# Optimization experiments

Measured on AMD Instinct MI355X. Metric: run time of the kernel, lower is better.

Reference implementation:

```python
import jax, jax.numpy as jnp
import numpy as np

# Irreps config: input/output = 32x0e + 16x1o (dim 80), H=4 heads -> head = 8x0e + 4x1o (dim 20)
M0, M1 = 32, 16      # input muls for 0e / 1o
m0, m1 = 8, 4        # per-head muls
H = 4
HEAD_DIM = m0 + 3 * m1   # 20
WNUM = H * (M0 * m0 + M1 * m0 + M0 * m1 + M1 * m1)  # 2304 per-edge TP weights
NB, HID = 16, 64
SQRT3 = np.float32(np.sqrt(3.0))
EPS = 1e-8


def radial_mlp(x, W1, b1, W2, b2):
    return jax.nn.silu(x @ W1 + b1) @ W2 + b2


def tp_edge(ss, vv, sh0, sh1, w):
    """FullyConnectedTensorProduct (32x0e+16x1o) x (1x0e+1x1o) -> H*(8x0e+4x1o) with per-edge weights w [E, WNUM].
    Paths: 0e*0e->0e, 1o*1o->0e (CG dot/sqrt3), 0e*1o->1o, 1o*0e->1o; path norm 1/sqrt(fan_in)."""
    E = ss.shape[0]
    per = M0 * m0 + M1 * m0 + M0 * m1 + M1 * m1  # 576
    w = w.reshape(E, H, per)
    o = 0
    Wss = w[..., o:o + M0 * m0].reshape(E, H, M0, m0); o += M0 * m0
    Wvv = w[..., o:o + M1 * m0].reshape(E, H, M1, m0); o += M1 * m0
    Wsv = w[..., o:o + M0 * m1].reshape(E, H, M0, m1); o += M0 * m1
    Wvs = w[..., o:o + M1 * m1].reshape(E, H, M1, m1)
    fan = np.float32(np.sqrt(M0 + M1))  # fan_in = 48 for both output irreps
    vv_dot = jnp.einsum('eui,ei->eu', vv, sh1) / SQRT3
    out0 = (jnp.einsum('eu,ehuw->ehw', ss * sh0[:, None], Wss)
            + jnp.einsum('eu,ehuw->ehw', vv_dot, Wvv)) / fan          # [E,H,m0]
    out1 = (jnp.einsum('eu,ehuw->ehw', ss, Wsv)[..., None] * sh1[:, None, None, :]
            + jnp.einsum('eui,ehuw->ehwi', vv * sh0[:, None, None], Wvs)) / fan  # [E,H,m1,3]
    return out0, out1


def setup_inputs() -> dict:
    key = jax.random.key(0)
    ks = jax.random.split(key, 24)
    N, E = 2000, 32000
    g = lambda k, s, sc=1.0: jax.random.normal(k, s, jnp.float32) * sc
    inp = {}
    inp['node_features'] = g(ks[0], (N, M0 + 3 * M1))
    inp['edge_index'] = jax.random.randint(ks[1], (2, E), 0, N)
    inp['edge_sh'] = g(ks[2], (E, 4))
    inp['edge_radial_emb'] = jax.random.uniform(ks[3], (E, NB), jnp.float32)
    # query e3nn Linear (per-head blocks)
    inp['Wq0'] = g(ks[4], (H, M0, m0))
    inp['Wq1'] = g(ks[5], (H, M1, m1))
    # radial MLPs for key / value TP weights
    inp['Wk1'] = g(ks[6], (NB, HID), 1 / np.sqrt(NB)); inp['bk1'] = jnp.zeros((HID,), jnp.float32)
    inp['Wk2'] = g(ks[7], (HID, WNUM), 1 / np.sqrt(HID)); inp['bk2'] = jnp.zeros((WNUM,), jnp.float32)
    inp['Wv1'] = g(ks[8], (NB, HID), 1 / np.sqrt(NB)); inp['bv1'] = jnp.zeros((HID,), jnp.float32)
    inp['Wv2'] = g(ks[9], (HID, WNUM), 1 / np.sqrt(HID)); inp['bv2'] = jnp.zeros((WNUM,), jnp.float32)
    # single-head dot-product TP -> 0e (shared weights)
    inp['Wd0'] = g(ks[10], (m0, m0))
    inp['Wd1'] = g(ks[11], (m1, m1))
    # output projection Linear (all heads mixed per irrep)
    inp['Wo0'] = g(ks[12], (H * m0, M0))
    inp['Wo1'] = g(ks[13], (H * m1, M1))
    # FFN: out irreps -> (2*M0)x0e + M1x1o -> out irreps
    inp['Wf1_0'] = g(ks[14], (M0, 2 * M0))
    inp['Wf1_1'] = g(ks[15], (M1, M1))
    inp['Wf2_0'] = g(ks[16], (2 * M0, M0))
    inp['Wf2_1'] = g(ks[17], (M1, M1))
    return inp


def reference(node_features, edge_index, edge_sh, edge_radial_emb,
              Wq0, Wq1, Wk1, bk1, Wk2, bk2, Wv1, bv1, Wv2, bv2,
              Wd0, Wd1, Wo0, Wo1, Wf1_0, Wf1_1, Wf2_0, Wf2_1):
    N = node_features.shape[0]
    s = node_features[:, :M0]                       # [N, M0] scalars
    v = node_features[:, M0:].reshape(N, M1, 3)     # [N, M1, 3] vectors
    src, dst = edge_index[0], edge_index[1]

    # query Linear (e3nn: per-irrep channel mix, norm 1/sqrt(fan_in))
    q0 = jnp.einsum('nu,huw->nhw', s, Wq0) / np.sqrt(M0)
    q1 = jnp.einsum('nui,huw->nhwi', v, Wq1) / np.sqrt(M1)

    sh0, sh1 = edge_sh[:, 0], edge_sh[:, 1:4]
    ss, vv = s[src], v[src]                         # gather per edge

    wk = radial_mlp(edge_radial_emb, Wk1, bk1, Wk2, bk2)
    wv = radial_mlp(edge_radial_emb, Wv1, bv1, Wv2, bv2)
    k0, k1 = tp_edge(ss, vv, sh0, sh1, wk)
    v0, v1 = tp_edge(ss, vv, sh0, sh1, wv)

    # per-head equivariant dot product -> 0e logits
    qd0, qd1 = q0[dst], q1[dst]
    fan_d = np.float32(np.sqrt(m0 * m0 + m1 * m1))
    logits = (jnp.einsum('ehu,uv,ehv->eh', qd0, Wd0, k0)
              + jnp.einsum('ehui,uv,ehvi->eh', qd1, Wd1, k1) / SQRT3) / fan_d
    logits = logits / np.sqrt(HEAD_DIM)             # self.scale
    logits = jnp.clip(logits, -10.0, 10.0)

    # scatter softmax over edges sharing a destination node
    seg_max = jax.ops.segment_max(logits, dst, num_segments=N)
    seg_max = jnp.maximum(seg_max, -10.0)           # handle empty segments
    ex = jnp.exp(logits - seg_max[dst])
    denom = jax.ops.segment_sum(ex, dst, num_segments=N)
    alpha = ex / (denom[dst] + 1e-12)               # [E, H]

    agg0 = jax.ops.segment_sum(alpha[..., None] * v0, dst, num_segments=N)        # [N,H,m0]
    agg1 = jax.ops.segment_sum(alpha[..., None, None] * v1, dst, num_segments=N)  # [N,H,m1,3]

    # output projection Linear over concatenated heads
    o0 = agg0.reshape(N, H * m0) @ Wo0 / np.sqrt(H * m0)
    o1 = jnp.einsum('nui,uw->nwi', agg1.reshape(N, H * m1, 3), Wo1) / np.sqrt(H * m1)

    # residual (input irreps == output irreps -> identity skip)
    x0 = s + o0
    x1 = v + o1

    # FFN with SafeNormActivation
    f0 = x0 @ Wf1_0 / np.sqrt(M0)                               # [N, 2*M0]
    f1 = jnp.einsum('nui,uw->nwi', x1, Wf1_1) / np.sqrt(M1)     # [N, M1, 3]
    a0 = jax.nn.silu(f0)
    norms = jnp.linalg.norm(f1, axis=-1, keepdims=True)
    safe = jnp.maximum(norms, EPS)
    a1 = jnp.where(norms < EPS, 0.0, (f1 / safe) * jax.nn.silu(norms))
    g0 = a0 @ Wf2_0 / np.sqrt(2 * M0)
    g1 = jnp.einsum('nui,uw->nwi', a1, Wf2_1) / np.sqrt(M1)

    out0 = x0 + g0
    out1 = x1 + g1
    return jnp.concatenate([out0, out1.reshape(N, M1 * 3)], axis=-1)
```

## Files before the change

kernel.cpp:

```cpp
#include <hip/hip_runtime.h>

typedef unsigned int uint;
typedef unsigned short ushort;
typedef __attribute__((ext_vector_type(8))) short bf16x8;
typedef __attribute__((ext_vector_type(4))) float f32x4;

#define N_NODES 2000
#define N_EDGES 32000
#define WNUM 2304

constexpr size_t OFF_AGG0 = 0;
constexpr size_t OFF_AGG1 = 64000;
constexpr size_t OFF_DEN  = 160000;
constexpr size_t OFF_FLAG = 168000;
constexpr size_t OFF_W2T  = 168004;
constexpr size_t OFF_QT0  = 315460;
constexpr size_t OFF_QT1  = 379460;

__device__ __forceinline__ float b2f(ushort u){ union{uint i; float f;}x; x.i=((uint)u)<<16; return x.f; }
__device__ __forceinline__ float lo16(uint w){ union{uint u; float f;}x; x.u=w<<16; return x.f; }
__device__ __forceinline__ float hi16(uint w){ union{uint u; float f;}x; x.u=w&0xFFFF0000u; return x.f; }
__device__ __forceinline__ ushort f2b(float f){
  union{float f; uint u;}x; x.f=f;
  uint r = (x.u + 0x7FFFu + ((x.u>>16)&1u)) >> 16;
  return (ushort)r;
}
__device__ __forceinline__ float siluf(float x){ return x / (1.f + __expf(-x)); }

template<bool F32>
__device__ __forceinline__ float ldf(const void* p, int i){
  if (F32) return ((const float*)p)[i];
  return b2f(((const ushort*)p)[i]);
}
__device__ __forceinline__ float ldfr(const void* p, int i, bool f32){
  return f32 ? ((const float*)p)[i] : b2f(((const ushort*)p)[i]);
}

template<bool F32>
__device__ void node_q_one(const void* __restrict__ nf,
    const void* __restrict__ Wq0, const void* __restrict__ Wq1,
    const void* __restrict__ Wd0, const void* __restrict__ Wd1,
    float* __restrict__ qt0, float* __restrict__ qt1, int tid){
  int n = tid >> 2, h = tid & 3;
  float s[32], v[48];
  #pragma unroll
  for (int u=0; u<32; ++u) s[u] = ldf<F32>(nf, n*80+u);
  #pragma unroll
  for (int u=0; u<48; ++u) v[u] = ldf<F32>(nf, n*80+32+u);
  float q0[8];
  #pragma unroll
  for (int w=0; w<8; ++w){
    float a = 0.f;
    #pragma unroll
    for (int u=0; u<32; ++u) a += s[u]*ldf<F32>(Wq0, h*256 + u*8 + w);
    q0[w] = a * 0.17677669529663687f;
  }
  #pragma unroll
  for (int vv=0; vv<8; ++vv){
    float a = 0.f;
    #pragma unroll
    for (int u=0; u<8; ++u) a += q0[u]*ldf<F32>(Wd0, u*8+vv);
    qt0[n*32 + h*8 + vv] = a;
  }
  float q1[12];
  #pragma unroll
  for (int w=0; w<4; ++w)
    #pragma unroll
    for (int i=0; i<3; ++i){
      float a = 0.f;
      #pragma unroll
      for (int u=0; u<16; ++u) a += v[u*3+i]*ldf<F32>(Wq1, h*64 + u*4 + w);
      q1[w*3+i] = a * 0.25f;
    }
  #pragma unroll
  for (int vv=0; vv<4; ++vv)
    #pragma unroll
    for (int i=0; i<3; ++i){
      float a = 0.f;
      #pragma unroll
      for (int u=0; u<4; ++u) a += q1[u*3+i]*ldf<F32>(Wd1, u*4+vv);
      qt1[n*48 + h*12 + vv*3 + i] = a;
    }
}

__global__ __launch_bounds__(256) void prep_kernel(
    const void* __restrict__ nf, const void* __restrict__ Wk2, const void* __restrict__ Wv2,
    const void* __restrict__ Wq0, const void* __restrict__ Wq1,
    const void* __restrict__ Wd0, const void* __restrict__ Wd1,
    ushort* __restrict__ W2T, float* __restrict__ qt0, float* __restrict__ qt1,
    float* __restrict__ aggz, int* __restrict__ flag){
  __shared__ int s_cnt;
  const int t = threadIdx.x;
  if (t == 0) s_cnt = 0;
  __syncthreads();
  {
    uint u = ((const ushort*)nf)[t*2];
    uint ex = (u >> 7) & 0xFFu;
    if (ex >= 0xA0u) atomicAdd(&s_cnt, 1);
  }
  __syncthreads();
  const bool F32 = (s_cnt >= 20);
  if (blockIdx.x == 0 && t == 0) *flag = F32 ? 1 : 0;

  if (blockIdx.x < 72){
    __shared__ ushort tile[64][66];
    const int b = blockIdx.x, mat = b / 36, jt = b - mat*36;
    const void* W = mat ? Wv2 : Wk2;
    const int j0 = jt*64;
    const int jo = t & 63, cb = t >> 6;
    #pragma unroll
    for (int k=0; k<16; ++k){
      const int c = cb + k*4;
      tile[c][jo] = F32 ? f2b(((const float*)W)[(size_t)c*WNUM + j0 + jo])
                        : ((const ushort*)W)[(size_t)c*WNUM + j0 + jo];
    }
    __syncthreads();
    const int jl = t >> 2, c0 = (t & 3)*16;
    ushort* dst = W2T + (size_t)mat*147456 + (size_t)(j0+jl)*64 + c0;
    #pragma unroll
    for (int k=0; k<16; ++k) dst[k] = tile[c0+k][jl];
  } else {
    const int zb = (int)blockIdx.x - 72;
    float4* az = (float4*)aggz;
    for (int idx = zb*256 + t; idx < 42000; idx += 32*256)
      az[idx] = make_float4(0.f,0.f,0.f,0.f);
    const int tid = zb*256 + t;
    if (tid < N_NODES*4){
      if (F32) node_q_one<true >(nf, Wq0, Wq1, Wd0, Wd1, qt0, qt1, tid);
      else     node_q_one<false>(nf, Wq0, Wq1, Wd0, Wd1, qt0, qt1, tid);
    }
  }
}

struct Smem {
  ushort hidA[2][32][72];
  float fssT[32][36];
  float fvvT[16][36];
  float sslT[32][36];
  float vshT[16][3][36];
  float sh1T[3][36];
  int   dstL[32];
};

template<bool F32>
__device__ void edge_body(
    const void* __restrict__ nf,  const int* __restrict__ eidx,
    const void* __restrict__ esh, const void* __restrict__ emb,
    const void* __restrict__ Wk1, const void* __restrict__ bk1, const void* __restrict__ bk2,
    const void* __restrict__ Wv1, const void* __restrict__ bv1, const void* __restrict__ bv2,
    const ushort* __restrict__ W2T,
    const float* __restrict__ qt0g, const float* __restrict__ qt1g,
    float* __restrict__ agg0, float* __restrict__ agg1, float* __restrict__ denom,
    Smem& sm){
  const int t  = threadIdx.x;
  const int hw = t >> 5;
  const int r  = t & 31;
  const int geb = blockIdx.x*32;

  #pragma unroll 1
  for (int e=0; e<4; ++e){
    const int le = hw*4+e, ge = geb+le;
    const int src = eidx[ge], d = eidx[N_EDGES+ge];
    const float sh0 = ldf<F32>(esh, ge*4+0);
    const float s1a = ldf<F32>(esh, ge*4+1), s1b = ldf<F32>(esh, ge*4+2), s1c = ldf<F32>(esh, ge*4+3);
    if (r == 0) sm.dstL[le] = d;
    if (r < 3) sm.sh1T[r][le] = (r==0)? s1a : (r==1)? s1b : s1c;
    float sv = ldf<F32>(nf, src*80 + r);
    sm.sslT[r][le] = sv;
    sm.fssT[r][le] = sv * sh0;
    if (r < 16){
      float v0 = ldf<F32>(nf, src*80+32+r*3+0);
      float v1 = ldf<F32>(nf, src*80+32+r*3+1);
      float v2 = ldf<F32>(nf, src*80+32+r*3+2);
      sm.vshT[r][0][le] = v0*sh0; sm.vshT[r][1][le] = v1*sh0; sm.vshT[r][2][le] = v2*sh0;
      sm.fvvT[r][le] = (v0*s1a + v1*s1b + v2*s1c) * 0.5773502691896258f;
    }
  }

  #pragma unroll 1
  for (int e=0; e<4; ++e){
    const int le = hw*4+e, ge = geb+le;
    float em[16];
    if (F32){
      const float4* p = (const float4*)((const float*)emb + ge*16);
      float4 a=p[0], b=p[1], c=p[2], d4=p[3];
      em[0]=a.x; em[1]=a.y; em[2]=a.z; em[3]=a.w;
      em[4]=b.x; em[5]=b.y; em[6]=b.z; em[7]=b.w;
      em[8]=c.x; em[9]=c.y; em[10]=c.z; em[11]=c.w;
      em[12]=d4.x; em[13]=d4.y; em[14]=d4.z; em[15]=d4.w;
    } else {
      const uint4* p = (const uint4*)((const ushort*)emb + ge*16);
      uint4 a=p[0], b=p[1];
      em[0]=lo16(a.x); em[1]=hi16(a.x); em[2]=lo16(a.y); em[3]=hi16(a.y);
      em[4]=lo16(a.z); em[5]=hi16(a.z); em[6]=lo16(a.w); em[7]=hi16(a.w);
      em[8]=lo16(b.x); em[9]=hi16(b.x); em[10]=lo16(b.y); em[11]=hi16(b.y);
      em[12]=lo16(b.z); em[13]=hi16(b.z); em[14]=lo16(b.w); em[15]=hi16(b.w);
    }
    #pragma unroll
    for (int cc=0; cc<2; ++cc){
      const int c = r + cc*32;
      float ak = ldf<F32>(bk1, c), av = ldf<F32>(bv1, c);
      #pragma unroll
      for (int b=0; b<16; ++b){
        ak += em[b] * ldf<F32>(Wk1, b*64 + c);
        av += em[b] * ldf<F32>(Wv1, b*64 + c);
      }
      sm.hidA[0][le][c] = f2b(siluf(ak));
      sm.hidA[1][le][c] = f2b(siluf(av));
    }
  }
  __syncthreads();

  const int h = t >> 6;
  const int lane = t & 63, q = lane >> 4, n = lane & 15;
  const ushort* w2tk = W2T;
  const ushort* w2tv = W2T + 147456;

  bf16x8 af[2][2][2];
  #pragma unroll
  for (int kv=0; kv<2; ++kv)
    #pragma unroll
    for (int Mt=0; Mt<2; ++Mt)
      #pragma unroll
      for (int kh=0; kh<2; ++kh)
        af[kv][Mt][kh] = *(const bf16x8*)&sm.hidA[kv][Mt*16+n][kh*32 + q*8];

  float aK0[2][4], aV0[2][4], aPK[2][4], aPV[2][4], aWK[3][2][4], aWV[3][2][4];
  #pragma unroll
  for (int Mt=0; Mt<2; ++Mt)
    #pragma unroll
    for (int z=0; z<4; ++z){
      aK0[Mt][z]=0.f; aV0[Mt][z]=0.f; aPK[Mt][z]=0.f; aPV[Mt][z]=0.f;
      aWK[0][Mt][z]=0.f; aWK[1][Mt][z]=0.f; aWK[2][Mt][z]=0.f;
      aWV[0][Mt][z]=0.f; aWV[1][Mt][z]=0.f; aWV[2][Mt][z]=0.f;
    }

  #pragma unroll 2
  for (int tl=0; tl<24; ++tl){
    const size_t tb = ((size_t)((h*36+tl)*16 + n))*64 + q*8;
    bf16x8 bk0 = *(const bf16x8*)(w2tk + tb), bk1f = *(const bf16x8*)(w2tk + tb + 32);
    bf16x8 bv0 = *(const bf16x8*)(w2tv + tb), bv1f = *(const bf16x8*)(w2tv + tb + 32);
    const int j = h*576 + tl*16 + n;
    const float bbk = ldf<F32>(bk2, j), bbv = ldf<F32>(bv2, j);
    const bool ss = (tl < 16);
    const int u = ss ? (tl*2 + (n>>3)) : ((tl-16)*2 + (n>>3));
    #pragma unroll
    for (int Mt=0; Mt<2; ++Mt){
      f32x4 fv = ss ? *(const f32x4*)&sm.fssT[u][Mt*16+q*4]
                    : *(const f32x4*)&sm.fvvT[u][Mt*16+q*4];
      f32x4 ck = {bbk,bbk,bbk,bbk};
      ck = __builtin_amdgcn_mfma_f32_16x16x32_bf16(af[0][Mt][0], bk0, ck, 0,0,0);
      ck = __builtin_amdgcn_mfma_f32_16x16x32_bf16(af[0][Mt][1], bk1f, ck, 0,0,0);
      f32x4 cv = {bbv,bbv,bbv,bbv};
      cv = __builtin_amdgcn_mfma_f32_16x16x32_bf16(af[1][Mt][0], bv0, cv, 0,0,0);
      cv = __builtin_amdgcn_mfma_f32_16x16x32_bf16(af[1][Mt][1], bv1f, cv, 0,0,0);
      #pragma unroll
      for (int z=0; z<4; ++z){ aK0[Mt][z] += ck[z]*fv[z]; aV0[Mt][z] += cv[z]*fv[z]; }
    }
  }
  #pragma unroll 2
  for (int tl=24; tl<32; ++tl){
    const size_t tb = ((size_t)((h*36+tl)*16 + n))*64 + q*8;
    bf16x8 bk0 = *(const bf16x8*)(w2tk + tb), bk1f = *(const bf16x8*)(w2tk + tb + 32);
    bf16x8 bv0 = *(const bf16x8*)(w2tv + tb), bv1f = *(const bf16x8*)(w2tv + tb + 32);
    const int j = h*576 + tl*16 + n;
    const float bbk = ldf<F32>(bk2, j), bbv = ldf<F32>(bv2, j);
    const int u = (tl-24)*4 + (n>>2);
    #pragma unroll
    for (int Mt=0; Mt<2; ++Mt){
      f32x4 fv = *(const f32x4*)&sm.sslT[u][Mt*16+q*4];
      f32x4 ck = {bbk,bbk,bbk,bbk};
      ck = __builtin_amdgcn_mfma_f32_16x16x32_bf16(af[0][Mt][0], bk0, ck, 0,0,0);
      ck = __builtin_amdgcn_mfma_f32_16x16x32_bf16(af[0][Mt][1], bk1f, ck, 0,0,0);
      f32x4 cv = {bbv,bbv,bbv,bbv};
      cv = __builtin_amdgcn_mfma_f32_16x16x32_bf16(af[1][Mt][0], bv0, cv, 0,0,0);
      cv = __builtin_amdgcn_mfma_f32_16x16x32_bf16(af[1][Mt][1], bv1f, cv, 0,0,0);
      #pragma unroll
      for (int z=0; z<4; ++z){ aPK[Mt][z] += ck[z]*fv[z]; aPV[Mt][z] += cv[z]*fv[z]; }
    }
  }
  #pragma unroll 1
  for (int tl=32; tl<36; ++tl){
    const size_t tb = ((size_t)((h*36+tl)*16 + n))*64 + q*8;
    bf16x8 bk0 = *(const bf16x8*)(w2tk + tb), bk1f = *(const bf16x8*)(w2tk + tb + 32);
    bf16x8 bv0 = *(const bf16x8*)(w2tv + tb), bv1f = *(const bf16x8*)(w2tv + tb + 32);
    const int j = h*576 + tl*16 + n;
    const float bbk = ldf<F32>(bk2, j), bbv = ldf<F32>(bv2, j);
    const int u = (tl-32)*4 + (n>>2);
    #pragma unroll
    for (int Mt=0; Mt<2; ++Mt){
      f32x4 ck = {bbk,bbk,bbk,bbk};
      ck = __builtin_amdgcn_mfma_f32_16x16x32_bf16(af[0][Mt][0], bk0, ck, 0,0,0);
      ck = __builtin_amdgcn_mfma_f32_16x16x32_bf16(af[0][Mt][1], bk1f, ck, 0,0,0);
      f32x4 cv = {bbv,bbv,bbv,bbv};
      cv = __builtin_amdgcn_mfma_f32_16x16x32_bf16(af[1][Mt][0], bv0, cv, 0,0,0);
      cv = __builtin_amdgcn_mfma_f32_16x16x32_bf16(af[1][Mt][1], bv1f, cv, 0,0,0);
      #pragma unroll
      for (int i=0; i<3; ++i){
        f32x4 fv = *(const f32x4*)&sm.vshT[u][i][Mt*16+q*4];
        #pragma unroll
        for (int z=0; z<4; ++z){ aWK[i][Mt][z] += ck[z]*fv[z]; aWV[i][Mt][z] += cv[z]*fv[z]; }
      }
    }
  }

  #pragma unroll
  for (int Mt=0; Mt<2; ++Mt)
    #pragma unroll
    for (int z=0; z<4; ++z){
      aK0[Mt][z] += __shfl_xor(aK0[Mt][z], 8, 64);
      aV0[Mt][z] += __shfl_xor(aV0[Mt][z], 8, 64);
      aPK[Mt][z] += __shfl_xor(aPK[Mt][z], 4, 64);
      aPK[Mt][z] += __shfl_xor(aPK[Mt][z], 8, 64);
      aPV[Mt][z] += __shfl_xor(aPV[Mt][z], 4, 64);
      aPV[Mt][z] += __shfl_xor(aPV[Mt][z], 8, 64);
      #pragma unroll
      for (int i=0; i<3; ++i){
        aWK[i][Mt][z] += __shfl_xor(aWK[i][Mt][z], 4, 64);
        aWK[i][Mt][z] += __shfl_xor(aWK[i][Mt][z], 8, 64);
        aWV[i][Mt][z] += __shfl_xor(aWV[i][Mt][z], 4, 64);
        aWV[i][Mt][z] += __shfl_xor(aWV[i][Mt][z], 8, 64);
      }
    }

  const float invfan = 0.14433756729740643f;
  int dn[2][4];
  #pragma unroll
  for (int Mt=0; Mt<2; ++Mt)
    #pragma unroll
    for (int z=0; z<4; ++z) dn[Mt][z] = sm.dstL[Mt*16 + q*4 + z];

  f32x4 s1v[3][2];
  #pragma unroll
  for (int i=0; i<3; ++i)
    #pragma unroll
    for (int Mt=0; Mt<2; ++Mt)
      s1v[i][Mt] = *(const f32x4*)&sm.sh1T[i][Mt*16+q*4];

  float lgp[2][4];
  #pragma unroll
  for (int Mt=0; Mt<2; ++Mt)
    #pragma unroll
    for (int z=0; z<4; ++z){
      float acc = 0.f;
      if (n < 8) acc = qt0g[dn[Mt][z]*32 + h*8 + n] * aK0[Mt][z];
      if (n < 4){
        float s = 0.f;
        #pragma unroll
        for (int i=0; i<3; ++i){
          float k1 = aPK[Mt][z]*s1v[i][Mt][z] + aWK[i][Mt][z];
          s += qt1g[dn[Mt][z]*48 + h*12 + n*3 + i] * k1;
        }
        acc += s * 0.5773502691896258f;
      }
      lgp[Mt][z] = acc;
    }
  #pragma unroll
  for (int Mt=0; Mt<2; ++Mt)
    #pragma unroll
    for (int z=0; z<4; ++z){
      lgp[Mt][z] += __shfl_xor(lgp[Mt][z], 1, 64);
      lgp[Mt][z] += __shfl_xor(lgp[Mt][z], 2, 64);
      lgp[Mt][z] += __shfl_xor(lgp[Mt][z], 4, 64);
      lgp[Mt][z] += __shfl_xor(lgp[Mt][z], 8, 64);
    }

  float exv[2][4];
  #pragma unroll
  for (int Mt=0; Mt<2; ++Mt)
    #pragma unroll
    for (int z=0; z<4; ++z){
      float lg = lgp[Mt][z] * invfan * 0.025f;
      lg = fminf(10.f, fmaxf(-10.f, lg));
      exv[Mt][z] = __expf(lg - 10.0f);
    }

  if (n == 0){
    #pragma unroll
    for (int Mt=0; Mt<2; ++Mt)
      #pragma unroll
      for (int z=0; z<4; ++z)
        atomicAdd(denom + dn[Mt][z]*4 + h, exv[Mt][z]);
  }
  if (n < 8){
    #pragma unroll
    for (int Mt=0; Mt<2; ++Mt)
      #pragma unroll
      for (int z=0; z<4; ++z)
        atomicAdd(agg0 + dn[Mt][z]*32 + h*8 + n, exv[Mt][z]*aV0[Mt][z]*invfan);
  }
  if (n < 4){
    #pragma unroll
    for (int i=0; i<3; ++i)
      #pragma unroll
      for (int Mt=0; Mt<2; ++Mt)
        #pragma unroll
        for (int z=0; z<4; ++z){
          float v1 = (aPV[Mt][z]*s1v[i][Mt][z] + aWV[i][Mt][z]) * invfan;
          atomicAdd(agg1 + dn[Mt][z]*48 + h*12 + n*3 + i, exv[Mt][z]*v1);
        }
  }
}

__global__ __launch_bounds__(256) void edge_kernel(
    const void* nf, const int* eidx, const void* esh, const void* emb,
    const void* Wk1, const void* bk1, const void* bk2,
    const void* Wv1, const void* bv1, const void* bv2,
    const ushort* W2T, const float* qt0g, const float* qt1g,
    float* agg0, float* agg1, float* denom, const int* flag){
  __shared__ Smem sm;
  if (*flag)
    edge_body<true >(nf,eidx,esh,emb,Wk1,bk1,bk2,Wv1,bv1,bv2,W2T,qt0g,qt1g,agg0,agg1,denom,sm);
  else
    edge_body<false>(nf,eidx,esh,emb,Wk1,bk1,bk2,Wv1,bv1,bv2,W2T,qt0g,qt1g,agg0,agg1,denom,sm);
}

__global__ __launch_bounds__(256) void node_out_kernel(
    const void* __restrict__ nf, const float* __restrict__ agg0r, const float* __restrict__ agg1r,
    const float* __restrict__ denom,
    const void* __restrict__ Wo0, const void* __restrict__ Wo1,
    const void* __restrict__ Wf10, const void* __restrict__ Wf11,
    const void* __restrict__ Wf20, const void* __restrict__ Wf21,
    void* __restrict__ out, const int* __restrict__ flag){
  __shared__ float ag0[4][32], ag1[4][48], adiv[4][4];
  __shared__ float x0s[4][32], x1s[4][48], a0s[4][64], f1s[4][48], coefs[4][16];
  const bool F32 = (*flag) != 0;
  const int g = threadIdx.x >> 6, t = threadIdx.x & 63;
  const int n = blockIdx.x*4 + g;
  if (t < 4) adiv[g][t] = 1.f / (denom[n*4+t] + 1e-12f);
  __syncthreads();
  if (t < 32) ag0[g][t] = agg0r[n*32+t] * adiv[g][t>>3];
  if (t < 48) ag1[g][t] = agg1r[n*48+t] * adiv[g][t/12];
  __syncthreads();
  if (t < 32){
    float o = 0.f;
    #pragma unroll
    for (int k=0; k<32; ++k) o += ag0[g][k]*ldfr(Wo0, k*32+t, F32);
    x0s[g][t] = ldfr(nf, n*80+t, F32) + o*0.17677669529663687f;
  }
  if (t < 48){
    int w = t/3, i = t - w*3;
    float o = 0.f;
    #pragma unroll
    for (int u=0; u<16; ++u) o += ag1[g][u*3+i]*ldfr(Wo1, u*16+w, F32);
    x1s[g][t] = ldfr(nf, n*80+32+t, F32) + o*0.25f;
  }
  __syncthreads();
  {
    float f0 = 0.f;
    #pragma unroll
    for (int u=0; u<32; ++u) f0 += x0s[g][u]*ldfr(Wf10, u*64+t, F32);
    a0s[g][t] = siluf(f0*0.17677669529663687f);
  }
  if (t < 48){
    int w = t/3, i = t - w*3;
    float f1 = 0.f;
    #pragma unroll
    for (int u=0; u<16; ++u) f1 += x1s[g][u*3+i]*ldfr(Wf11, u*16+w, F32);
    f1s[g][t] = f1*0.25f;
  }
  __syncthreads();
  if (t < 16){
    float a = f1s[g][t*3], b = f1s[g][t*3+1], c = f1s[g][t*3+2];
    float nrm = sqrtf(a*a+b*b+c*c);
    float safe = fmaxf(nrm, 1e-8f);
    coefs[g][t] = (nrm < 1e-8f) ? 0.f : siluf(nrm)/safe;
  }
  __syncthreads();
  if (t < 32){
    float gg = 0.f;
    #pragma unroll
    for (int u=0; u<64; ++u) gg += a0s[g][u]*ldfr(Wf20, u*32+t, F32);
    float val = x0s[g][t] + gg*0.125f;
    if (F32) ((float*)out)[n*80+t] = val; else ((ushort*)out)[n*80+t] = f2b(val);
  }
  if (t < 48){
    int w = t/3, i = t - w*3;
    float gg = 0.f;
    #pragma unroll
    for (int u=0; u<16; ++u) gg += coefs[g][u]*f1s[g][u*3+i]*ldfr(Wf21, u*16+w, F32);
    float val = x1s[g][t] + gg*0.25f;
    if (F32) ((float*)out)[n*80+32+t] = val; else ((ushort*)out)[n*80+32+t] = f2b(val);
  }
}

extern "C" void kernel_launch(void* const* d_in, const int* in_sizes, int n_in,
                              void* d_out, int out_size, void* d_ws, size_t ws_size,
                              hipStream_t stream){
  const void* nf   = d_in[0];
  const int*  eidx = (const int*)d_in[1];
  const void* esh  = d_in[2];
  const void* emb  = d_in[3];
  const void* Wq0  = d_in[4];
  const void* Wq1  = d_in[5];
  const void* Wk1  = d_in[6];
  const void* bk1  = d_in[7];
  const void* Wk2  = d_in[8];
  const void* bk2  = d_in[9];
  const void* Wv1  = d_in[10];
  const void* bv1  = d_in[11];
  const void* Wv2  = d_in[12];
  const void* bv2  = d_in[13];
  const void* Wd0  = d_in[14];
  const void* Wd1  = d_in[15];
  const void* Wo0  = d_in[16];
  const void* Wo1  = d_in[17];
  const void* Wf10 = d_in[18];
  const void* Wf11 = d_in[19];
  const void* Wf20 = d_in[20];
  const void* Wf21 = d_in[21];
  float* ws = (float*)d_ws;

  float* agg0  = ws + OFF_AGG0;
  float* agg1  = ws + OFF_AGG1;
  float* denom = ws + OFF_DEN;
  int*   flag  = (int*)(ws + OFF_FLAG);
  ushort* W2T  = (ushort*)(ws + OFF_W2T);
  float* qt0   = ws + OFF_QT0;
  float* qt1   = ws + OFF_QT1;

  prep_kernel<<<104, 256, 0, stream>>>(nf, Wk2, Wv2, Wq0, Wq1, Wd0, Wd1,
                                       W2T, qt0, qt1, agg0, flag);
  edge_kernel<<<N_EDGES/32, 256, 0, stream>>>(nf, eidx, esh, emb,
                                              Wk1, bk1, bk2, Wv1, bv1, bv2,
                                              W2T, qt0, qt1,
                                              agg0, agg1, denom, flag);
  node_out_kernel<<<N_NODES/4, 256, 0, stream>>>(nf, agg0, agg1, denom,
                                                 Wo0, Wo1, Wf10, Wf11, Wf20, Wf21, d_out, flag);
}
```

Baseline: 242.1 us.

## Sort edges by destination and segment-reduce contributions in shared memory before atomics

Adds a counting sort of edges by destination (count, scan, scatter kernels) and has the edge kernel process edges in that order. Per-edge softmax numerators and weighted values are staged in shared memory and run-length reduced over consecutive equal destinations, so one atomic is issued per destination run instead of one per edge. The node output kernel is also reshaped to one 64-thread block per node. This adds three small launches and an extra sync plus a serial 32-step reduction per block, in exchange for far fewer global atomics.

After: 239.3 us. No clear change (-1.2%).

```diff
diff --git a/kernel.cpp b/kernel.cpp
--- a/kernel.cpp
+++ b/kernel.cpp
@@ -16,6 +16,8 @@
 constexpr size_t OFF_W2T  = 168004;
 constexpr size_t OFF_QT0  = 315460;
 constexpr size_t OFF_QT1  = 379460;
+constexpr size_t OFF_CNT  = 475460;
+constexpr size_t OFF_EORD = 477460;
 
 __device__ __forceinline__ float b2f(ushort u){ union{uint i; float f;}x; x.i=((uint)u)<<16; return x.f; }
 __device__ __forceinline__ float lo16(uint w){ union{uint u; float f;}x; x.u=w<<16; return x.f; }
@@ -88,7 +90,7 @@
     const void* __restrict__ Wq0, const void* __restrict__ Wq1,
     const void* __restrict__ Wd0, const void* __restrict__ Wd1,
     ushort* __restrict__ W2T, float* __restrict__ qt0, float* __restrict__ qt1,
-    float* __restrict__ aggz, int* __restrict__ flag){
+    float* __restrict__ aggz, int* __restrict__ cnt, int* __restrict__ flag){
   __shared__ int s_cnt;
   const int t = threadIdx.x;
   if (t == 0) s_cnt = 0;
@@ -124,11 +126,46 @@
     float4* az = (float4*)aggz;
     for (int idx = zb*256 + t; idx < 42000; idx += 32*256)
       az[idx] = make_float4(0.f,0.f,0.f,0.f);
+    for (int idx = zb*256 + t; idx < N_NODES; idx += 32*256)
+      cnt[idx] = 0;
     const int tid = zb*256 + t;
     if (tid < N_NODES*4){
       if (F32) node_q_one<true >(nf, Wq0, Wq1, Wd0, Wd1, qt0, qt1, tid);
       else     node_q_one<false>(nf, Wq0, Wq1, Wd0, Wd1, qt0, qt1, tid);
     }
+  }
+}
+
+__global__ __launch_bounds__(256) void cnt_kernel(const int* __restrict__ eidx, int* __restrict__ cnt){
+  int e = blockIdx.x*256 + threadIdx.x;
+  if (e < N_EDGES) atomicAdd(cnt + eidx[N_EDGES + e], 1);
+}
+
+__global__ __launch_bounds__(256) void scan_kernel(int* __restrict__ cnt){
+  __shared__ int ls[256];
+  const int t = threadIdx.x;
+  const int base = t*8;
+  int v[8]; int s = 0;
+  #pragma unroll
+  for (int k=0; k<8; ++k){ int idx = base+k; v[k] = (idx < N_NODES) ? cnt[idx] : 0; s += v[k]; }
+  ls[t] = s; __syncthreads();
+  for (int off=1; off<256; off<<=1){
+    int x = (t >= off) ? ls[t-off] : 0;
+    __syncthreads();
+    ls[t] += x;
+    __syncthreads();
+  }
+  int ex = ls[t] - s;
+  #pragma unroll
+  for (int k=0; k<8; ++k){ int idx = base+k; if (idx < N_NODES){ int c = v[k]; cnt[idx] = ex; ex += c; } }
+}
+
+__global__ __launch_bounds__(256) void scat_kernel(const int* __restrict__ eidx,
+                                                   int* __restrict__ cnt, int* __restrict__ eord){
+  int e = blockIdx.x*256 + threadIdx.x;
+  if (e < N_EDGES){
+    int p = atomicAdd(cnt + eidx[N_EDGES + e], 1);
+    eord[p] = e;
   }
 }
 
@@ -139,12 +176,14 @@
   float sslT[32][36];
   float vshT[16][3][36];
   float sh1T[3][36];
+  float cont[4][32][21];
   int   dstL[32];
 };
 
 template<bool F32>
 __device__ void edge_body(
     const void* __restrict__ nf,  const int* __restrict__ eidx,
+    const int* __restrict__ eord,
     const void* __restrict__ esh, const void* __restrict__ emb,
     const void* __restrict__ Wk1, const void* __restrict__ bk1, const void* __restrict__ bk2,
     const void* __restrict__ Wv1, const void* __restrict__ bv1, const void* __restrict__ bv2,
@@ -159,7 +198,8 @@
 
   #pragma unroll 1
   for (int e=0; e<4; ++e){
-    const int le = hw*4+e, ge = geb+le;
+    const int le = hw*4+e;
+    const int ge = eord[geb+le];
     const int src = eidx[ge], d = eidx[N_EDGES+ge];
     const float sh0 = ldf<F32>(esh, ge*4+0);
     const float s1a = ldf<F32>(esh, ge*4+1), s1b = ldf<F32>(esh, ge*4+2), s1c = ldf<F32>(esh, ge*4+3);
@@ -179,7 +219,8 @@
 
   #pragma unroll 1
   for (int e=0; e<4; ++e){
-    const int le = hw*4+e, ge = geb+le;
+    const int le = hw*4+e;
+    const int ge = eord[geb+le];
     float em[16];
     if (F32){
       const float4* p = (const float4*)((const float*)emb + ge*16);
@@ -365,121 +406,120 @@
       lgp[Mt][z] += __shfl_xor(lgp[Mt][z], 8, 64);
     }
 
-  float exv[2][4];
   #pragma unroll
   for (int Mt=0; Mt<2; ++Mt)
     #pragma unroll
     for (int z=0; z<4; ++z){
       float lg = lgp[Mt][z] * invfan * 0.025f;
       lg = fminf(10.f, fmaxf(-10.f, lg));
-      exv[Mt][z] = __expf(lg - 10.0f);
-    }
-
-  if (n == 0){
-    #pragma unroll
-    for (int Mt=0; Mt<2; ++Mt)
-      #pragma unroll
-      for (int z=0; z<4; ++z)
-        atomicAdd(denom + dn[Mt][z]*4 + h, exv[Mt][z]);
-  }
-  if (n < 8){
-    #pragma unroll
-    for (int Mt=0; Mt<2; ++Mt)
-      #pragma unroll
-      for (int z=0; z<4; ++z)
-        atomicAdd(agg0 + dn[Mt][z]*32 + h*8 + n, exv[Mt][z]*aV0[Mt][z]*invfan);
-  }
-  if (n < 4){
-    #pragma unroll
-    for (int i=0; i<3; ++i)
-      #pragma unroll
-      for (int Mt=0; Mt<2; ++Mt)
+      const float ex = __expf(lg - 10.0f);
+      const int el = Mt*16 + q*4 + z;
+      if (n == 0) sm.cont[h][el][0] = ex;
+      if (n < 8)  sm.cont[h][el][1+n] = ex * aV0[Mt][z] * invfan;
+      if (n < 4){
         #pragma unroll
-        for (int z=0; z<4; ++z){
+        for (int i=0; i<3; ++i){
           float v1 = (aPV[Mt][z]*s1v[i][Mt][z] + aWV[i][Mt][z]) * invfan;
-          atomicAdd(agg1 + dn[Mt][z]*48 + h*12 + n*3 + i, exv[Mt][z]*v1);
+          sm.cont[h][el][9+n*3+i] = ex * v1;
         }
+      }
+    }
+  __syncthreads();
+
+  if (t < 84){
+    const int h2 = t / 21, comp = t - h2*21;
+    float acc = 0.f;
+    #pragma unroll 1
+    for (int e2=0; e2<32; ++e2){
+      acc += sm.cont[h2][e2][comp];
+      const int d2 = sm.dstL[e2];
+      if (e2 == 31 || sm.dstL[e2+1] != d2){
+        if (comp == 0)      atomicAdd(denom + d2*4  + h2, acc);
+        else if (comp < 9)  atomicAdd(agg0  + d2*32 + h2*8  + (comp-1), acc);
+        else                atomicAdd(agg1  + d2*48 + h2*12 + (comp-9), acc);
+        acc = 0.f;
+      }
+    }
   }
 }
 
 __global__ __launch_bounds__(256) void edge_kernel(
-    const void* nf, const int* eidx, const void* esh, const void* emb,
+    const void* nf, const int* eidx, const int* eord, const void* esh, const void* emb,
     const void* Wk1, const void* bk1, const void* bk2,
     const void* Wv1, const void* bv1, const void* bv2,
     const ushort* W2T, const float* qt0g, const float* qt1g,
     float* agg0, float* agg1, float* denom, const int* flag){
   __shared__ Smem sm;
   if (*flag)
-    edge_body<true >(nf,eidx,esh,emb,Wk1,bk1,bk2,Wv1,bv1,bv2,W2T,qt0g,qt1g,agg0,agg1,denom,sm);
+    edge_body<true >(nf,eidx,eord,esh,emb,Wk1,bk1,bk2,Wv1,bv1,bv2,W2T,qt0g,qt1g,agg0,agg1,denom,sm);
   else
-    edge_body<false>(nf,eidx,esh,emb,Wk1,bk1,bk2,Wv1,bv1,bv2,W2T,qt0g,qt1g,agg0,agg1,denom,sm);
-}
-
-__global__ __launch_bounds__(256) void node_out_kernel(
+    edge_body<false>(nf,eidx,eord,esh,emb,Wk1,bk1,bk2,Wv1,bv1,bv2,W2T,qt0g,qt1g,agg0,agg1,denom,sm);
+}
+
+__global__ __launch_bounds__(64) void node_out_kernel(
     const void* __restrict__ nf, const float* __restrict__ agg0r, const float* __restrict__ agg1r,
     const float* __restrict__ denom,
     const void* __restrict__ Wo0, const void* __restrict__ Wo1,
     const void* __restrict__ Wf10, const void* __restrict__ Wf11,
     const void* __restrict__ Wf20, const void* __restrict__ Wf21,
     void* __restrict__ out, const int* __restrict__ flag){
-  __shared__ float ag0[4][32], ag1[4][48], adiv[4][4];
-  __shared__ float x0s[4][32], x1s[4][48], a0s[4][64], f1s[4][48], coefs[4][16];
+  __shared__ float ag0[32], ag1[48], adiv[4];
+  __shared__ float x0s[32], x1s[48], a0s[64], f1s[48], coefs[16];
   const bool F32 = (*flag) != 0;
-  const int g = threadIdx.x >> 6, t = threadIdx.x & 63;
-  const int n = blockIdx.x*4 + g;
-  if (t < 4) adiv[g][t] = 1.f / (denom[n*4+t] + 1e-12f);
-  __syncthreads();
-  if (t < 32) ag0[g][t] = agg0r[n*32+t] * adiv[g][t>>3];
-  if (t < 48) ag1[g][t] = agg1r[n*48+t] * adiv[g][t/12];
+  const int n = blockIdx.x, t = threadIdx.x;
+  if (t < 4) adiv[t] = 1.f / (denom[n*4+t] + 1e-12f);
+  __syncthreads();
+  if (t < 32) ag0[t] = agg0r[n*32+t] * adiv[t>>3];
+  if (t < 48) ag1[t] = agg1r[n*48+t] * adiv[t/12];
   __syncthreads();
   if (t < 32){
     float o = 0.f;
     #pragma unroll
-    for (int k=0; k<32; ++k) o += ag0[g][k]*ldfr(Wo0, k*32+t, F32);
-    x0s[g][t] = ldfr(nf, n*80+t, F32) + o*0.17677669529663687f;
+    for (int k=0; k<32; ++k) o += ag0[k]*ldfr(Wo0, k*32+t, F32);
+    x0s[t] = ldfr(nf, n*80+t, F32) + o*0.17677669529663687f;
   }
   if (t < 48){
     int w = t/3, i = t - w*3;
     float o = 0.f;
     #pragma unroll
-    for (int u=0; u<16; ++u) o += ag1[g][u*3+i]*ldfr(Wo1, u*16+w, F32);
-    x1s[g][t] = ldfr(nf, n*80+32+t, F32) + o*0.25f;
+    for (int u=0; u<16; ++u) o += ag1[u*3+i]*ldfr(Wo1, u*16+w, F32);
+    x1s[t] = ldfr(nf, n*80+32+t, F32) + o*0.25f;
   }
   __syncthreads();
   {
     float f0 = 0.f;
     #pragma unroll
-    for (int u=0; u<32; ++u) f0 += x0s[g][u]*ldfr(Wf10, u*64+t, F32);
-    a0s[g][t] = siluf(f0*0.17677669529663687f);
+    for (int u=0; u<32; ++u) f0 += x0s[u]*ldfr(Wf10, u*64+t, F32);
+    a0s[t] = siluf(f0*0.17677669529663687f);
   }
   if (t < 48){
     int w = t/3, i = t - w*3;
     float f1 = 0.f;
     #pragma unroll
-    for (int u=0; u<16; ++u) f1 += x1s[g][u*3+i]*ldfr(Wf11, u*16+w, F32);
-    f1s[g][t] = f1*0.25f;
+    for (int u=0; u<16; ++u) f1 += x1s[u*3+i]*ldfr(Wf11, u*16+w, F32);
+    f1s[t] = f1*0.25f;
   }
   __syncthreads();
   if (t < 16){
-    float a = f1s[g][t*3], b = f1s[g][t*3+1], c = f1s[g][t*3+2];
+    float a = f1s[t*3], b = f1s[t*3+1], c = f1s[t*3+2];
     float nrm = sqrtf(a*a+b*b+c*c);
     float safe = fmaxf(nrm, 1e-8f);
-    coefs[g][t] = (nrm < 1e-8f) ? 0.f : siluf(nrm)/safe;
+    coefs[t] = (nrm < 1e-8f) ? 0.f : siluf(nrm)/safe;
   }
   __syncthreads();
   if (t < 32){
-    float gg = 0.f;
-    #pragma unroll
-    for (int u=0; u<64; ++u) gg += a0s[g][u]*ldfr(Wf20, u*32+t, F32);
-    float val = x0s[g][t] + gg*0.125f;
+    float g = 0.f;
+    #pragma unroll
+    for (int u=0; u<64; ++u) g += a0s[u]*ldfr(Wf20, u*32+t, F32);
+    float val = x0s[t] + g*0.125f;
     if (F32) ((float*)out)[n*80+t] = val; else ((ushort*)out)[n*80+t] = f2b(val);
   }
   if (t < 48){
     int w = t/3, i = t - w*3;
-    float gg = 0.f;
-    #pragma unroll
-    for (int u=0; u<16; ++u) gg += coefs[g][u]*f1s[g][u*3+i]*ldfr(Wf21, u*16+w, F32);
-    float val = x1s[g][t] + gg*0.25f;
+    float g = 0.f;
+    #pragma unroll
+    for (int u=0; u<16; ++u) g += coefs[u]*f1s[u*3+i]*ldfr(Wf21, u*16+w, F32);
+    float val = x1s[t] + g*0.25f;
     if (F32) ((float*)out)[n*80+32+t] = val; else ((ushort*)out)[n*80+32+t] = f2b(val);
   }
 }
@@ -518,13 +558,18 @@
   ushort* W2T  = (ushort*)(ws + OFF_W2T);
   float* qt0   = ws + OFF_QT0;
   float* qt1   = ws + OFF_QT1;
+  int*   cnt   = (int*)(ws + OFF_CNT);
+  int*   eord  = (int*)(ws + OFF_EORD);
 
   prep_kernel<<<104, 256, 0, stream>>>(nf, Wk2, Wv2, Wq0, Wq1, Wd0, Wd1,
-                                       W2T, qt0, qt1, agg0, flag);
-  edge_kernel<<<N_EDGES/32, 256, 0, stream>>>(nf, eidx, esh, emb,
+                                       W2T, qt0, qt1, agg0, cnt, flag);
+  cnt_kernel<<<125, 256, 0, stream>>>(eidx, cnt);
+  scan_kernel<<<1, 256, 0, stream>>>(cnt);
+  scat_kernel<<<125, 256, 0, stream>>>(eidx, cnt, eord);
+  edge_kernel<<<N_EDGES/32, 256, 0, stream>>>(nf, eidx, eord, esh, emb,
                                               Wk1, bk1, bk2, Wv1, bv1, bv2,
                                               W2T, qt0, qt1,
                                               agg0, agg1, denom, flag);
-  node_out_kernel<<<N_NODES/4, 256, 0, stream>>>(nf, agg0, agg1, denom,
-                                                 Wo0, Wo1, Wf10, Wf11, Wf20, Wf21, d_out, flag);
-}
+  node_out_kernel<<<N_NODES, 64, 0, stream>>>(nf, agg0, agg1, denom,
+                                              Wo0, Wo1, Wf10, Wf11, Wf20, Wf21, d_out, flag);
+}
```
